# Kernel optimization log

Hardware: AMD Instinct MI355X
Metric: run time of the kernel (lower is better)

Reference implementation:

```python
import jax, jax.numpy as jnp
import numpy as np

N_NODES = 50000
N_EDGES = 800000
N_GRAPHS = 512
NODE_IN = 128
EDGE_IN = 64
HIDDEN = 128
SHARED = 64


def setup_inputs() -> dict:
    key = jax.random.key(0)
    ks = jax.random.split(key, 24)
    def lin(k, fan_in, fan_out):
        lim = 1.0 / np.sqrt(fan_in)
        kw, kb = jax.random.split(k)
        w = jax.random.uniform(kw, (fan_in, fan_out), jnp.float32, -lim, lim)
        b = jax.random.uniform(kb, (fan_out,), jnp.float32, -lim, lim)
        return w, b
    x = jax.random.normal(ks[0], (N_NODES, NODE_IN), jnp.float32)
    edge_index = jax.random.randint(ks[1], (2, N_EDGES), 0, N_NODES, jnp.int64)
    edge_attr = jax.random.normal(ks[2], (N_EDGES, EDGE_IN), jnp.float32)
    batch = jnp.sort(jax.random.randint(ks[3], (N_NODES,), 0, N_GRAPHS, jnp.int64))
    e1_w, e1_b = lin(ks[4], EDGE_IN, NODE_IN)
    n1_w1, n1_b1 = lin(ks[5], NODE_IN, HIDDEN)
    n1_w2, n1_b2 = lin(ks[6], HIDDEN, HIDDEN)
    e2_w, e2_b = lin(ks[7], EDGE_IN, HIDDEN)
    n2_w1, n2_b1 = lin(ks[8], HIDDEN, HIDDEN)
    n2_w2, n2_b2 = lin(ks[9], HIDDEN, HIDDEN)
    fc_w, fc_b = lin(ks[10], HIDDEN, SHARED)
    hS_w, hS_b = lin(ks[11], SHARED, 1)
    hP_w, hP_b = lin(ks[12], SHARED, 1)
    hN_w, hN_b = lin(ks[13], SHARED, 1)
    return dict(x=x, edge_index=edge_index, edge_attr=edge_attr, batch=batch,
                e1_w=e1_w, e1_b=e1_b, n1_w1=n1_w1, n1_b1=n1_b1, n1_w2=n1_w2, n1_b2=n1_b2,
                e2_w=e2_w, e2_b=e2_b, n2_w1=n2_w1, n2_b1=n2_b1, n2_w2=n2_w2, n2_b2=n2_b2,
                fc_w=fc_w, fc_b=fc_b, hS_w=hS_w, hS_b=hS_b, hP_w=hP_w, hP_b=hP_b,
                hN_w=hN_w, hN_b=hN_b)


def gine_conv(x, edge_index, edge_attr, ew, eb, w1, b1, w2, b2):
    # message: relu(x_j + Lin(edge_attr)); aggregate: scatter-sum to target;
    # update: MLP((1 + eps) * x_i + aggr) with eps = 0 (PyG default)
    e = edge_attr @ ew + eb                      # [E, C]
    m = jax.nn.relu(x[edge_index[0]] + e)        # gather + fused add/relu
    aggr = jax.ops.segment_sum(m, edge_index[1], num_segments=N_NODES)
    h = x + aggr
    return jax.nn.relu(h @ w1 + b1) @ w2 + b2


def global_mean_pool(x, batch):
    sums = jax.ops.segment_sum(x, batch, num_segments=N_GRAPHS)
    cnt = jax.ops.segment_sum(jnp.ones((x.shape[0],), x.dtype), batch, num_segments=N_GRAPHS)
    return sums / jnp.maximum(cnt, 1.0)[:, None]


def reference(x, edge_index, edge_attr, batch,
              e1_w, e1_b, n1_w1, n1_b1, n1_w2, n1_b2,
              e2_w, e2_b, n2_w1, n2_b1, n2_w2, n2_b2,
              fc_w, fc_b, hS_w, hS_b, hP_w, hP_b, hN_w, hN_b):
    h = jax.nn.relu(gine_conv(x, edge_index, edge_attr, e1_w, e1_b, n1_w1, n1_b1, n1_w2, n1_b2))
    h = jax.nn.relu(gine_conv(h, edge_index, edge_attr, e2_w, e2_b, n2_w1, n2_b1, n2_w2, n2_b2))
    g = global_mean_pool(h, batch)               # [G, HIDDEN]
    s = jax.nn.relu(g @ fc_w + fc_b)             # [G, SHARED]
    logS = (s @ hS_w + hS_b)[:, 0]
    logP = (s @ hP_w + hP_b)[:, 0]
    nr = (s @ hN_w + hN_b)[:, 0]
    return logS, logP, nr
```

## Files before the change

kernel.cpp:

```cpp
#include <hip/hip_runtime.h>
#include <hip/hip_bf16.h>


typedef __bf16 bf16_t;

#define N_NODES   50000
#define N_EDGES   800000
#define N_GRAPHS  512
#define HID       128
#define EIN       64

#define RL(v, l) __int_as_float(__builtin_amdgcn_readlane(__float_as_int(v), (l)))

__device__ __forceinline__ float ldf(const void* p, size_t i, int f32m) {
    return f32m ? ((const float*)p)[i] : (float)((const bf16_t*)p)[i];
}
__device__ __forceinline__ int ldi(const void* p, size_t i, int i64m) {
    return i64m ? (int)((const long long*)p)[i] : ((const int*)p)[i];
}

__global__ void k_detect(const unsigned short* __restrict__ xw,
                         const unsigned int*   __restrict__ eiw,
                         int* __restrict__ flags)
{
    if (threadIdx.x == 0 && blockIdx.x == 0) {
        int sane = 0;
        for (int i = 0; i < 256; ++i) {
            int e = (xw[i] >> 7) & 0xFF;
            if (e >= 100 && e <= 150) ++sane;
        }
        flags[0] = (sane < 220) ? 1 : 0;
        int nzhigh = 0;
        for (int i = 0; i < 256; ++i)
            if (eiw[2*i + 1] != 0) ++nzhigh;
        flags[1] = (nzhigh == 0) ? 1 : 0;
    }
}

__global__ void k_cvt4(const void* __restrict__ x, float* __restrict__ dst,
                       const int* __restrict__ flags) {
    const int f32m = flags[0];
    size_t i = (size_t)blockIdx.x * 256 + threadIdx.x;
    if (f32m) {
        ((float4*)dst)[i] = ((const float4*)x)[i];
    } else {
        const bf16_t* s = (const bf16_t*)x;
        float4 v;
        v.x = (float)s[4*i+0]; v.y = (float)s[4*i+1];
        v.z = (float)s[4*i+2]; v.w = (float)s[4*i+3];
        ((float4*)dst)[i] = v;
    }
}

__global__ __launch_bounds__(512) void k_edge_s(
        const void* __restrict__ Xg, int xg_ws,
        const void* __restrict__ ei,
        const void* __restrict__ ea,
        const void* __restrict__ ew,
        const void* __restrict__ eb,
        float*      __restrict__ ag,
        const int*  __restrict__ flags)
{
    __shared__ float4 Wq[16 * 128];
    __shared__ float  ebs[HID];
    const int f32m = flags[0];
    const int i64m = flags[1];
    const int xgf  = xg_ws ? 1 : f32m;

    for (int i = threadIdx.x; i < 16 * 128; i += 512) {
        int k4 = i >> 7, c = i & 127;
        float4 w;
        w.x = ldf(ew, (size_t)(4*k4+0)*HID + c, f32m);
        w.y = ldf(ew, (size_t)(4*k4+1)*HID + c, f32m);
        w.z = ldf(ew, (size_t)(4*k4+2)*HID + c, f32m);
        w.w = ldf(ew, (size_t)(4*k4+3)*HID + c, f32m);
        Wq[i] = w;
    }
    for (int i = threadIdx.x; i < HID; i += 512) ebs[i] = ldf(eb, i, f32m);
    __syncthreads();

    const int lane = threadIdx.x & 63;
    const int wid  = (blockIdx.x * 512 + threadIdx.x) >> 6;
    const int nw   = gridDim.x * 8;
    const int ngrp = N_EDGES / 8;

    for (int g = wid; g < ngrp; g += nw) {
        const int e0 = g * 8;
        float av[8]; int src[8], dst[8];
#pragma unroll
        for (int i = 0; i < 8; ++i) {
            av[i]  = ldf(ea, (size_t)(e0+i) * EIN + lane, f32m);
            src[i] = ldi(ei, e0+i, i64m);
            dst[i] = ldi(ei, (size_t)N_EDGES + e0+i, i64m);
        }
        float acc0[8], acc1[8];
#pragma unroll
        for (int i = 0; i < 8; ++i) { acc0[i] = 0.f; acc1[i] = 0.f; }

#pragma unroll 4
        for (int k4 = 0; k4 < 16; ++k4) {
            float4 w0 = Wq[k4 * 128 + lane];
            float4 w1 = Wq[k4 * 128 + 64 + lane];
#pragma unroll
            for (int i = 0; i < 8; ++i) {
                float a0 = RL(av[i], 4*k4+0);
                float a1 = RL(av[i], 4*k4+1);
                float a2 = RL(av[i], 4*k4+2);
                float a3 = RL(av[i], 4*k4+3);
                acc0[i] = fmaf(a3, w0.w, fmaf(a2, w0.z, fmaf(a1, w0.y, fmaf(a0, w0.x, acc0[i]))));
                acc1[i] = fmaf(a3, w1.w, fmaf(a2, w1.z, fmaf(a1, w1.y, fmaf(a0, w1.x, acc1[i]))));
            }
        }

#pragma unroll
        for (int i = 0; i < 8; ++i) {
            float x0 = ldf(Xg, (size_t)src[i] * HID + lane,      xgf);
            float x1 = ldf(Xg, (size_t)src[i] * HID + 64 + lane, xgf);
            float v0 = fmaxf(x0 + acc0[i] + ebs[lane],      0.f);
            float v1 = fmaxf(x1 + acc1[i] + ebs[64 + lane], 0.f);
            unsafeAtomicAdd(ag + (size_t)dst[i] * HID + lane,      v0);
            unsafeAtomicAdd(ag + (size_t)dst[i] * HID + 64 + lane, v1);
        }
    }
}

__global__ __launch_bounds__(1024) void k_mlp_s(
        const float* __restrict__ A,
        const void*  __restrict__ W,
        const void*  __restrict__ bias,
        float*       __restrict__ Out,
        float*       __restrict__ Out2,
        const int*   __restrict__ flags)
{
    __shared__ float4 Wq[32 * 128];
    const int f32m = flags[0];
    for (int i = threadIdx.x; i < 32 * 128; i += 1024) {
        int k4 = i >> 7, c = i & 127;
        float4 w;
        w.x = ldf(W, (size_t)(4*k4+0)*HID + c, f32m);
        w.y = ldf(W, (size_t)(4*k4+1)*HID + c, f32m);
        w.z = ldf(W, (size_t)(4*k4+2)*HID + c, f32m);
        w.w = ldf(W, (size_t)(4*k4+3)*HID + c, f32m);
        Wq[i] = w;
    }
    __syncthreads();

    const int lane = threadIdx.x & 63;
    const int wid  = (blockIdx.x * 1024 + threadIdx.x) >> 6;
    const int nw   = gridDim.x * 16;
    const float b0 = ldf(bias, lane,      f32m);
    const float b1 = ldf(bias, 64 + lane, f32m);
    const int ngrp = N_NODES / 8;

    for (int g = wid; g < ngrp; g += nw) {
        const int n0 = g * 8;
        float alo[8], ahi[8], acc0[8], acc1[8];
#pragma unroll
        for (int i = 0; i < 8; ++i) {
            alo[i] = A[(size_t)(n0+i) * HID + lane];
            ahi[i] = A[(size_t)(n0+i) * HID + 64 + lane];
            acc0[i] = b0; acc1[i] = b1;
        }
#pragma unroll 4
        for (int k4 = 0; k4 < 16; ++k4) {
            float4 w0 = Wq[k4 * 128 + lane];
            float4 w1 = Wq[k4 * 128 + 64 + lane];
#pragma unroll
            for (int i = 0; i < 8; ++i) {
                float a0 = RL(alo[i], 4*k4+0);
                float a1 = RL(alo[i], 4*k4+1);
                float a2 = RL(alo[i], 4*k4+2);
                float a3 = RL(alo[i], 4*k4+3);
                acc0[i] = fmaf(a3, w0.w, fmaf(a2, w0.z, fmaf(a1, w0.y, fmaf(a0, w0.x, acc0[i]))));
                acc1[i] = fmaf(a3, w1.w, fmaf(a2, w1.z, fmaf(a1, w1.y, fmaf(a0, w1.x, acc1[i]))));
            }
        }
#pragma unroll 4
        for (int k4 = 16; k4 < 32; ++k4) {
            float4 w0 = Wq[k4 * 128 + lane];
            float4 w1 = Wq[k4 * 128 + 64 + lane];
#pragma unroll
            for (int i = 0; i < 8; ++i) {
                float a0 = RL(ahi[i], 4*k4+0 - 64);
                float a1 = RL(ahi[i], 4*k4+1 - 64);
                float a2 = RL(ahi[i], 4*k4+2 - 64);
                float a3 = RL(ahi[i], 4*k4+3 - 64);
                acc0[i] = fmaf(a3, w0.w, fmaf(a2, w0.z, fmaf(a1, w0.y, fmaf(a0, w0.x, acc0[i]))));
                acc1[i] = fmaf(a3, w1.w, fmaf(a2, w1.z, fmaf(a1, w1.y, fmaf(a0, w1.x, acc1[i]))));
            }
        }
#pragma unroll
        for (int i = 0; i < 8; ++i) {
            float v0 = fmaxf(acc0[i], 0.f);
            float v1 = fmaxf(acc1[i], 0.f);
            Out[(size_t)(n0+i) * HID + lane]      = v0;
            Out[(size_t)(n0+i) * HID + 64 + lane] = v1;
            if (Out2) {
                Out2[(size_t)(n0+i) * HID + lane]      = v0;
                Out2[(size_t)(n0+i) * HID + 64 + lane] = v1;
            }
        }
    }
}

__global__ void k_pool_s(const float* __restrict__ X, const void* __restrict__ batch,
                         float* __restrict__ GS, float* __restrict__ GC,
                         const int* __restrict__ flags)
{
    const int i64m = flags[1];
    const int c  = threadIdx.x;
    const int n0 = blockIdx.x * 64;
    const int nend = (n0 + 64 < N_NODES) ? n0 + 64 : N_NODES;

    int bprev = ldi(batch, n0, i64m);
    float acc = 0.f;
    int   cnt = 0;
    for (int n = n0; n < nend; ++n) {
        int b = ldi(batch, n, i64m);
        if (b != bprev) {
            unsafeAtomicAdd(&GS[(size_t)bprev * HID + c], acc);
            if (c == 0) unsafeAtomicAdd(&GC[bprev], (float)cnt);
            acc = 0.f; cnt = 0; bprev = b;
        }
        acc += X[(size_t)n * HID + c];
        ++cnt;
    }
    unsafeAtomicAdd(&GS[(size_t)bprev * HID + c], acc);
    if (c == 0) unsafeAtomicAdd(&GC[bprev], (float)cnt);
}

__global__ void k_head(const float* __restrict__ GS, const float* __restrict__ GC,
                       const void* __restrict__ fcw, const void* __restrict__ fcb,
                       const void* __restrict__ hSw, const void* __restrict__ hSb,
                       const void* __restrict__ hPw, const void* __restrict__ hPb,
                       const void* __restrict__ hNw, const void* __restrict__ hNb,
                       float* __restrict__ out, const int* __restrict__ flags)
{
    const int f32m = flags[0];
    const int g = blockIdx.x;
    const int lane = threadIdx.x;
    const float inv = 1.f / fmaxf(GC[g], 1.f);
    const float g0 = GS[(size_t)g * HID + lane]      * inv;
    const float g1 = GS[(size_t)g * HID + 64 + lane] * inv;

    float acc = 0.f;
    for (int k = 0; k < 64; ++k) {
        float gk = __shfl(g0, k, 64);
        acc += gk * ldf(fcw, k * 64 + lane, f32m);
    }
    for (int k = 0; k < 64; ++k) {
        float gk = __shfl(g1, k, 64);
        acc += gk * ldf(fcw, (64 + k) * 64 + lane, f32m);
    }
    float s = fmaxf(acc + ldf(fcb, lane, f32m), 0.f);

    float pS = s * ldf(hSw, lane, f32m);
    float pP = s * ldf(hPw, lane, f32m);
    float pN = s * ldf(hNw, lane, f32m);
#pragma unroll
    for (int off = 32; off; off >>= 1) {
        pS += __shfl_down(pS, off, 64);
        pP += __shfl_down(pP, off, 64);
        pN += __shfl_down(pN, off, 64);
    }
    if (lane == 0) {
        out[g]                = pS + ldf(hSb, 0, f32m);
        out[N_GRAPHS + g]     = pP + ldf(hPb, 0, f32m);
        out[2 * N_GRAPHS + g] = pN + ldf(hNb, 0, f32m);
    }
}

extern "C" void kernel_launch(void* const* d_in, const int* in_sizes, int n_in,
                              void* d_out, int out_size, void* d_ws, size_t ws_size,
                              hipStream_t stream)
{
    const void* x     = d_in[0];
    const void* ei    = d_in[1];
    const void* ea    = d_in[2];
    const void* batch = d_in[3];
    const void* e1w = d_in[4],  *e1b = d_in[5];
    const void* n1w1= d_in[6],  *n1b1= d_in[7];
    const void* n1w2= d_in[8],  *n1b2= d_in[9];
    const void* e2w = d_in[10], *e2b = d_in[11];
    const void* n2w1= d_in[12], *n2b1= d_in[13];
    const void* n2w2= d_in[14], *n2b2= d_in[15];
    const void* fcw = d_in[16], *fcb = d_in[17];
    const void* hSw = d_in[18], *hSb = d_in[19];
    const void* hPw = d_in[20], *hPb = d_in[21];
    const void* hNw = d_in[22], *hNb = d_in[23];

    float* B1 = (float*)d_ws;
    float* B2 = B1 + (size_t)N_NODES * HID;
    float* GS = B2 + (size_t)N_NODES * HID;
    float* GC = GS + (size_t)N_GRAPHS * HID;
    int*   FL = (int*)(GC + N_GRAPHS);

    k_detect<<<1, 64, 0, stream>>>((const unsigned short*)x, (const unsigned int*)ei, FL);
    hipMemsetAsync(GS, 0, (N_GRAPHS * HID + N_GRAPHS) * sizeof(float), stream);

    const int NV4_BLKS = (N_NODES * HID / 4) / 256;

    k_cvt4  <<<NV4_BLKS, 256, 0, stream>>>(x, B1, FL);
    k_edge_s<<<1024, 512, 0, stream>>>(x, 0, ei, ea, e1w, e1b, B1, FL);
    k_mlp_s <<<512, 1024, 0, stream>>>(B1, n1w1, n1b1, B1, nullptr, FL);
    k_mlp_s <<<512, 1024, 0, stream>>>(B1, n1w2, n1b2, B1, B2, FL);

    k_edge_s<<<1024, 512, 0, stream>>>(B1, 1, ei, ea, e2w, e2b, B2, FL);
    k_mlp_s <<<512, 1024, 0, stream>>>(B2, n2w1, n2b1, B2, nullptr, FL);
    k_mlp_s <<<512, 1024, 0, stream>>>(B2, n2w2, n2b2, B2, nullptr, FL);

    k_pool_s<<<(N_NODES + 63) / 64, 128, 0, stream>>>(B2, batch, GS, GC, FL);
    k_head  <<<N_GRAPHS, 64, 0, stream>>>(GS, GC, fcw, fcb, hSw, hSb, hPw, hPb, hNw, hNb,
                                          (float*)d_out, FL);
}
```

Before: 1.283 ms.

## Replace atomic edge scatter with CSR-by-destination gather aggregation

Builds a destination-sorted CSR (histogram, three-stage scan, scatter of edge id and source) each call, then aggregates messages per node in registers and writes each node row once. This removes the float atomics on the aggregation buffer, the x-to-buffer conversion kernel and the duplicate output copy in the MLP. In exchange it adds several small preprocessing kernels with int atomics, random gathers of edge_attr rows through an indirection, and wave-level load imbalance from varying node degree.

```diff
diff --git a/kernel.cpp b/kernel.cpp
--- a/kernel.cpp
+++ b/kernel.cpp
@@ -9,6 +9,8 @@
 #define N_GRAPHS  512
 #define HID       128
 #define EIN       64
+#define SCAN_BLK  1024
+#define NCHUNK    49
 
 #define RL(v, l) __int_as_float(__builtin_amdgcn_readlane(__float_as_int(v), (l)))
 
@@ -37,34 +39,84 @@
     }
 }
 
-__global__ void k_cvt4(const void* __restrict__ x, float* __restrict__ dst,
-                       const int* __restrict__ flags) {
-    const int f32m = flags[0];
-    size_t i = (size_t)blockIdx.x * 256 + threadIdx.x;
-    if (f32m) {
-        ((float4*)dst)[i] = ((const float4*)x)[i];
-    } else {
-        const bf16_t* s = (const bf16_t*)x;
-        float4 v;
-        v.x = (float)s[4*i+0]; v.y = (float)s[4*i+1];
-        v.z = (float)s[4*i+2]; v.w = (float)s[4*i+3];
-        ((float4*)dst)[i] = v;
-    }
-}
-
-__global__ __launch_bounds__(512) void k_edge_s(
+__global__ void k_hist(const void* __restrict__ ei, int* __restrict__ CNT,
+                       const int* __restrict__ flags)
+{
+    const int i64m = flags[1];
+    int e = blockIdx.x * 256 + threadIdx.x;
+    int d = ldi(ei, (size_t)N_EDGES + e, i64m);
+    atomicAdd(&CNT[d], 1);
+}
+
+__global__ __launch_bounds__(SCAN_BLK) void k_scanA(const int* __restrict__ CNT,
+                                                    int* __restrict__ OFF,
+                                                    int* __restrict__ PS)
+{
+    __shared__ int tmp[SCAN_BLK];
+    const int t = threadIdx.x;
+    const int i = blockIdx.x * SCAN_BLK + t;
+    const int v = (i < N_NODES) ? CNT[i] : 0;
+    tmp[t] = v;
+    __syncthreads();
+    for (int off = 1; off < SCAN_BLK; off <<= 1) {
+        int u = (t >= off) ? tmp[t - off] : 0;
+        __syncthreads();
+        tmp[t] += u;
+        __syncthreads();
+    }
+    if (i < N_NODES) OFF[i] = tmp[t] - v;
+    if (t == SCAN_BLK - 1) PS[blockIdx.x] = tmp[t];
+}
+
+__global__ void k_scanB(int* __restrict__ PS)
+{
+    const int lane = threadIdx.x;
+    const int v0 = (lane < NCHUNK) ? PS[lane] : 0;
+    int v = v0;
+#pragma unroll
+    for (int off = 1; off < 64; off <<= 1) {
+        int u = __shfl_up(v, off, 64);
+        if (lane >= off) v += u;
+    }
+    if (lane < NCHUNK) PS[lane] = v - v0;
+}
+
+__global__ void k_scanC(int* __restrict__ OFF, const int* __restrict__ PS,
+                        int* __restrict__ CUR)
+{
+    int i = blockIdx.x * 256 + threadIdx.x;
+    if (i < N_NODES) {
+        int o = OFF[i] + PS[i >> 10];
+        OFF[i] = o;
+        CUR[i] = o;
+    }
+}
+
+__global__ void k_scatter(const void* __restrict__ ei, int* __restrict__ CUR,
+                          int2* __restrict__ ES, const int* __restrict__ flags)
+{
+    const int i64m = flags[1];
+    int e = blockIdx.x * 256 + threadIdx.x;
+    int s = ldi(ei, e, i64m);
+    int d = ldi(ei, (size_t)N_EDGES + e, i64m);
+    int p = atomicAdd(&CUR[d], 1);
+    ES[p] = make_int2(e, s);
+}
+
+__global__ __launch_bounds__(512) void k_edge_csr(
         const void* __restrict__ Xg, int xg_ws,
-        const void* __restrict__ ei,
+        const int2* __restrict__ ES,
+        const int*  __restrict__ OFF,
+        const int*  __restrict__ CNT,
         const void* __restrict__ ea,
         const void* __restrict__ ew,
         const void* __restrict__ eb,
-        float*      __restrict__ ag,
+        float*      __restrict__ out,
         const int*  __restrict__ flags)
 {
     __shared__ float4 Wq[16 * 128];
     __shared__ float  ebs[HID];
     const int f32m = flags[0];
-    const int i64m = flags[1];
     const int xgf  = xg_ws ? 1 : f32m;
 
     for (int i = threadIdx.x; i < 16 * 128; i += 512) {
@@ -82,45 +134,53 @@
     const int lane = threadIdx.x & 63;
     const int wid  = (blockIdx.x * 512 + threadIdx.x) >> 6;
     const int nw   = gridDim.x * 8;
-    const int ngrp = N_EDGES / 8;
-
-    for (int g = wid; g < ngrp; g += nw) {
-        const int e0 = g * 8;
-        float av[8]; int src[8], dst[8];
-#pragma unroll
-        for (int i = 0; i < 8; ++i) {
-            av[i]  = ldf(ea, (size_t)(e0+i) * EIN + lane, f32m);
-            src[i] = ldi(ei, e0+i, i64m);
-            dst[i] = ldi(ei, (size_t)N_EDGES + e0+i, i64m);
-        }
-        float acc0[8], acc1[8];
-#pragma unroll
-        for (int i = 0; i < 8; ++i) { acc0[i] = 0.f; acc1[i] = 0.f; }
+    const float eb0 = ebs[lane], eb1 = ebs[64 + lane];
+
+    for (int n = wid; n < N_NODES; n += nw) {
+        const int st = OFF[n];
+        const int d  = CNT[n];
+        float a0 = ldf(Xg, (size_t)n * HID + lane,      xgf);
+        float a1 = ldf(Xg, (size_t)n * HID + 64 + lane, xgf);
+
+        for (int base = 0; base < d; base += 8) {
+            const int m = d - base;
+            float av[8]; int src[8];
+#pragma unroll
+            for (int i = 0; i < 8; ++i) {
+                int2 es = ES[st + base + ((i < m) ? i : 0)];
+                src[i] = es.y;
+                av[i]  = ldf(ea, (size_t)es.x * EIN + lane, f32m);
+            }
+            float macc0[8], macc1[8];
+#pragma unroll
+            for (int i = 0; i < 8; ++i) { macc0[i] = 0.f; macc1[i] = 0.f; }
 
 #pragma unroll 4
-        for (int k4 = 0; k4 < 16; ++k4) {
-            float4 w0 = Wq[k4 * 128 + lane];
-            float4 w1 = Wq[k4 * 128 + 64 + lane];
+            for (int k4 = 0; k4 < 16; ++k4) {
+                float4 w0 = Wq[k4 * 128 + lane];
+                float4 w1 = Wq[k4 * 128 + 64 + lane];
+#pragma unroll
+                for (int i = 0; i < 8; ++i) {
+                    float a0b = RL(av[i], 4*k4+0);
+                    float a1b = RL(av[i], 4*k4+1);
+                    float a2b = RL(av[i], 4*k4+2);
+                    float a3b = RL(av[i], 4*k4+3);
+                    macc0[i] = fmaf(a3b, w0.w, fmaf(a2b, w0.z, fmaf(a1b, w0.y, fmaf(a0b, w0.x, macc0[i]))));
+                    macc1[i] = fmaf(a3b, w1.w, fmaf(a2b, w1.z, fmaf(a1b, w1.y, fmaf(a0b, w1.x, macc1[i]))));
+                }
+            }
 #pragma unroll
             for (int i = 0; i < 8; ++i) {
-                float a0 = RL(av[i], 4*k4+0);
-                float a1 = RL(av[i], 4*k4+1);
-                float a2 = RL(av[i], 4*k4+2);
-                float a3 = RL(av[i], 4*k4+3);
-                acc0[i] = fmaf(a3, w0.w, fmaf(a2, w0.z, fmaf(a1, w0.y, fmaf(a0, w0.x, acc0[i]))));
-                acc1[i] = fmaf(a3, w1.w, fmaf(a2, w1.z, fmaf(a1, w1.y, fmaf(a0, w1.x, acc1[i]))));
-            }
-        }
-
-#pragma unroll
-        for (int i = 0; i < 8; ++i) {
-            float x0 = ldf(Xg, (size_t)src[i] * HID + lane,      xgf);
-            float x1 = ldf(Xg, (size_t)src[i] * HID + 64 + lane, xgf);
-            float v0 = fmaxf(x0 + acc0[i] + ebs[lane],      0.f);
-            float v1 = fmaxf(x1 + acc1[i] + ebs[64 + lane], 0.f);
-            unsafeAtomicAdd(ag + (size_t)dst[i] * HID + lane,      v0);
-            unsafeAtomicAdd(ag + (size_t)dst[i] * HID + 64 + lane, v1);
-        }
+                if (i < m) {
+                    float x0 = ldf(Xg, (size_t)src[i] * HID + lane,      xgf);
+                    float x1 = ldf(Xg, (size_t)src[i] * HID + 64 + lane, xgf);
+                    a0 += fmaxf(x0 + macc0[i] + eb0, 0.f);
+                    a1 += fmaxf(x1 + macc1[i] + eb1, 0.f);
+                }
+            }
+        }
+        out[(size_t)n * HID + lane]      = a0;
+        out[(size_t)n * HID + 64 + lane] = a1;
     }
 }
 
@@ -129,7 +189,6 @@
         const void*  __restrict__ W,
         const void*  __restrict__ bias,
         float*       __restrict__ Out,
-        float*       __restrict__ Out2,
         const int*   __restrict__ flags)
 {
     __shared__ float4 Wq[32 * 128];
@@ -191,14 +250,8 @@
         }
 #pragma unroll
         for (int i = 0; i < 8; ++i) {
-            float v0 = fmaxf(acc0[i], 0.f);
-            float v1 = fmaxf(acc1[i], 0.f);
-            Out[(size_t)(n0+i) * HID + lane]      = v0;
-            Out[(size_t)(n0+i) * HID + 64 + lane] = v1;
-            if (Out2) {
-                Out2[(size_t)(n0+i) * HID + lane]      = v0;
-                Out2[(size_t)(n0+i) * HID + 64 + lane] = v1;
-            }
+            Out[(size_t)(n0+i) * HID + lane]      = fmaxf(acc0[i], 0.f);
+            Out[(size_t)(n0+i) * HID + 64 + lane] = fmaxf(acc1[i], 0.f);
         }
     }
 }
@@ -289,25 +342,34 @@
     const void* hPw = d_in[20], *hPb = d_in[21];
     const void* hNw = d_in[22], *hNb = d_in[23];
 
-    float* B1 = (float*)d_ws;
-    float* B2 = B1 + (size_t)N_NODES * HID;
-    float* GS = B2 + (size_t)N_NODES * HID;
-    float* GC = GS + (size_t)N_GRAPHS * HID;
-    int*   FL = (int*)(GC + N_GRAPHS);
+    float* B1  = (float*)d_ws;
+    float* B2  = B1 + (size_t)N_NODES * HID;
+    float* GS  = B2 + (size_t)N_NODES * HID;
+    float* GC  = GS + (size_t)N_GRAPHS * HID;
+    int*   FL  = (int*)(GC + N_GRAPHS);
+    int*   PS  = FL + 4;
+    int*   OFF = PS + 64;
+    int*   CNT = OFF + N_NODES;
+    int*   CUR = CNT + N_NODES;
+    int2*  ES  = (int2*)(CUR + N_NODES);
 
     k_detect<<<1, 64, 0, stream>>>((const unsigned short*)x, (const unsigned int*)ei, FL);
     hipMemsetAsync(GS, 0, (N_GRAPHS * HID + N_GRAPHS) * sizeof(float), stream);
-
-    const int NV4_BLKS = (N_NODES * HID / 4) / 256;
-
-    k_cvt4  <<<NV4_BLKS, 256, 0, stream>>>(x, B1, FL);
-    k_edge_s<<<1024, 512, 0, stream>>>(x, 0, ei, ea, e1w, e1b, B1, FL);
-    k_mlp_s <<<512, 1024, 0, stream>>>(B1, n1w1, n1b1, B1, nullptr, FL);
-    k_mlp_s <<<512, 1024, 0, stream>>>(B1, n1w2, n1b2, B1, B2, FL);
-
-    k_edge_s<<<1024, 512, 0, stream>>>(B1, 1, ei, ea, e2w, e2b, B2, FL);
-    k_mlp_s <<<512, 1024, 0, stream>>>(B2, n2w1, n2b1, B2, nullptr, FL);
-    k_mlp_s <<<512, 1024, 0, stream>>>(B2, n2w2, n2b2, B2, nullptr, FL);
+    hipMemsetAsync(CNT, 0, N_NODES * sizeof(int), stream);
+
+    k_hist   <<<N_EDGES / 256, 256, 0, stream>>>(ei, CNT, FL);
+    k_scanA  <<<NCHUNK, SCAN_BLK, 0, stream>>>(CNT, OFF, PS);
+    k_scanB  <<<1, 64, 0, stream>>>(PS);
+    k_scanC  <<<(N_NODES + 255) / 256, 256, 0, stream>>>(OFF, PS, CUR);
+    k_scatter<<<N_EDGES / 256, 256, 0, stream>>>(ei, CUR, ES, FL);
+
+    k_edge_csr<<<1024, 512, 0, stream>>>(x, 0, ES, OFF, CNT, ea, e1w, e1b, B1, FL);
+    k_mlp_s   <<<512, 1024, 0, stream>>>(B1, n1w1, n1b1, B1, FL);
+    k_mlp_s   <<<512, 1024, 0, stream>>>(B1, n1w2, n1b2, B1, FL);
+
+    k_edge_csr<<<1024, 512, 0, stream>>>(B1, 1, ES, OFF, CNT, ea, e2w, e2b, B2, FL);
+    k_mlp_s   <<<512, 1024, 0, stream>>>(B2, n2w1, n2b1, B2, FL);
+    k_mlp_s   <<<512, 1024, 0, stream>>>(B2, n2w2, n2b2, B2, FL);
 
     k_pool_s<<<(N_NODES + 63) / 64, 128, 0, stream>>>(B2, batch, GS, GC, FL);
     k_head  <<<N_GRAPHS, 64, 0, stream>>>(GS, GC, fcw, fcb, hSw, hSb, hPw, hPb, hNw, hNb,
```

After: 1.614 ms. 25.8% more time.

## Software-pipeline edge kernel loads, broadcast indices via readlane, shrink pool chunks

Applied to the files above, without the earlier changes.

The edge kernel now prefetches the next edge group's attributes and indices while computing the current one. Instead of every lane loading all 16 indices, one lane per index loads it and readlane broadcasts it. The source-node gathers are issued before the matmul so their latency overlaps the FMAs, and the edge grid doubles to 2048 blocks. The pool kernel uses 16-node chunks with lane-loaded batch ids, giving more blocks at the cost of extra register pressure and more atomics.

```diff
diff --git a/kernel.cpp b/kernel.cpp
--- a/kernel.cpp
+++ b/kernel.cpp
@@ -9,8 +9,10 @@
 #define N_GRAPHS  512
 #define HID       128
 #define EIN       64
-
-#define RL(v, l) __int_as_float(__builtin_amdgcn_readlane(__float_as_int(v), (l)))
+#define PNODES    16
+
+#define RL(v, l)  __int_as_float(__builtin_amdgcn_readlane(__float_as_int(v), (l)))
+#define RLI(v, l) __builtin_amdgcn_readlane((v), (l))
 
 __device__ __forceinline__ float ldf(const void* p, size_t i, int f32m) {
     return f32m ? ((const float*)p)[i] : (float)((const bf16_t*)p)[i];
@@ -83,43 +85,86 @@
     const int wid  = (blockIdx.x * 512 + threadIdx.x) >> 6;
     const int nw   = gridDim.x * 8;
     const int ngrp = N_EDGES / 8;
-
-    for (int g = wid; g < ngrp; g += nw) {
-        const int e0 = g * 8;
-        float av[8]; int src[8], dst[8];
-#pragma unroll
-        for (int i = 0; i < 8; ++i) {
-            av[i]  = ldf(ea, (size_t)(e0+i) * EIN + lane, f32m);
-            src[i] = ldi(ei, e0+i, i64m);
-            dst[i] = ldi(ei, (size_t)N_EDGES + e0+i, i64m);
-        }
-        float acc0[8], acc1[8];
-#pragma unroll
-        for (int i = 0; i < 8; ++i) { acc0[i] = 0.f; acc1[i] = 0.f; }
+    const float eb0 = ebs[lane], eb1 = ebs[64 + lane];
+
+    auto LOADIDX = [&](int e0) -> int {
+        int v = 0;
+        if (lane < 16) {
+            size_t idx = (lane < 8) ? (size_t)(e0 + lane)
+                                    : (size_t)N_EDGES + (e0 + lane - 8);
+            v = ldi(ei, idx, i64m);
+        }
+        return v;
+    };
+
+    int g = wid;
+    if (g < ngrp) {
+        float avA[8]; int vvA;
+        {
+            const int e0 = g * 8;
+            vvA = LOADIDX(e0);
+#pragma unroll
+            for (int i = 0; i < 8; ++i)
+                avA[i] = ldf(ea, (size_t)(e0+i) * EIN + lane, f32m);
+        }
+
+        while (true) {
+            const int gB = g + nw;
+            const bool hasB = (gB < ngrp);
+            float avB[8]; int vvB = 0;
+            if (hasB) {
+                const int e0B = gB * 8;
+                vvB = LOADIDX(e0B);
+#pragma unroll
+                for (int i = 0; i < 8; ++i)
+                    avB[i] = ldf(ea, (size_t)(e0B+i) * EIN + lane, f32m);
+            }
+
+            int src[8], dst[8];
+#pragma unroll
+            for (int i = 0; i < 8; ++i) {
+                src[i] = RLI(vvA, i);
+                dst[i] = RLI(vvA, 8 + i);
+            }
+            float x0[8], x1[8];
+#pragma unroll
+            for (int i = 0; i < 8; ++i) {
+                x0[i] = ldf(Xg, (size_t)src[i] * HID + lane,      xgf);
+                x1[i] = ldf(Xg, (size_t)src[i] * HID + 64 + lane, xgf);
+            }
+
+            float acc0[8], acc1[8];
+#pragma unroll
+            for (int i = 0; i < 8; ++i) { acc0[i] = 0.f; acc1[i] = 0.f; }
 
 #pragma unroll 4
-        for (int k4 = 0; k4 < 16; ++k4) {
-            float4 w0 = Wq[k4 * 128 + lane];
-            float4 w1 = Wq[k4 * 128 + 64 + lane];
-#pragma unroll
-            for (int i = 0; i < 8; ++i) {
-                float a0 = RL(av[i], 4*k4+0);
-                float a1 = RL(av[i], 4*k4+1);
-                float a2 = RL(av[i], 4*k4+2);
-                float a3 = RL(av[i], 4*k4+3);
-                acc0[i] = fmaf(a3, w0.w, fmaf(a2, w0.z, fmaf(a1, w0.y, fmaf(a0, w0.x, acc0[i]))));
-                acc1[i] = fmaf(a3, w1.w, fmaf(a2, w1.z, fmaf(a1, w1.y, fmaf(a0, w1.x, acc1[i]))));
-            }
-        }
-
-#pragma unroll
-        for (int i = 0; i < 8; ++i) {
-            float x0 = ldf(Xg, (size_t)src[i] * HID + lane,      xgf);
-            float x1 = ldf(Xg, (size_t)src[i] * HID + 64 + lane, xgf);
-            float v0 = fmaxf(x0 + acc0[i] + ebs[lane],      0.f);
-            float v1 = fmaxf(x1 + acc1[i] + ebs[64 + lane], 0.f);
-            unsafeAtomicAdd(ag + (size_t)dst[i] * HID + lane,      v0);
-            unsafeAtomicAdd(ag + (size_t)dst[i] * HID + 64 + lane, v1);
+            for (int k4 = 0; k4 < 16; ++k4) {
+                float4 w0 = Wq[k4 * 128 + lane];
+                float4 w1 = Wq[k4 * 128 + 64 + lane];
+#pragma unroll
+                for (int i = 0; i < 8; ++i) {
+                    float a0 = RL(avA[i], 4*k4+0);
+                    float a1 = RL(avA[i], 4*k4+1);
+                    float a2 = RL(avA[i], 4*k4+2);
+                    float a3 = RL(avA[i], 4*k4+3);
+                    acc0[i] = fmaf(a3, w0.w, fmaf(a2, w0.z, fmaf(a1, w0.y, fmaf(a0, w0.x, acc0[i]))));
+                    acc1[i] = fmaf(a3, w1.w, fmaf(a2, w1.z, fmaf(a1, w1.y, fmaf(a0, w1.x, acc1[i]))));
+                }
+            }
+
+#pragma unroll
+            for (int i = 0; i < 8; ++i) {
+                float v0 = fmaxf(x0[i] + acc0[i] + eb0, 0.f);
+                float v1 = fmaxf(x1[i] + acc1[i] + eb1, 0.f);
+                unsafeAtomicAdd(ag + (size_t)dst[i] * HID + lane,      v0);
+                unsafeAtomicAdd(ag + (size_t)dst[i] * HID + 64 + lane, v1);
+            }
+
+            if (!hasB) break;
+            g = gB;
+            vvA = vvB;
+#pragma unroll
+            for (int i = 0; i < 8; ++i) avA[i] = avB[i];
         }
     }
 }
@@ -209,20 +254,23 @@
 {
     const int i64m = flags[1];
     const int c  = threadIdx.x;
-    const int n0 = blockIdx.x * 64;
-    const int nend = (n0 + 64 < N_NODES) ? n0 + 64 : N_NODES;
-
-    int bprev = ldi(batch, n0, i64m);
+    const int tl = threadIdx.x & 63;
+    const int n0 = blockIdx.x * PNODES;
+
+    int bv = (tl < PNODES) ? ldi(batch, n0 + tl, i64m) : 0;
+
+    int bprev = RLI(bv, 0);
     float acc = 0.f;
     int   cnt = 0;
-    for (int n = n0; n < nend; ++n) {
-        int b = ldi(batch, n, i64m);
+#pragma unroll
+    for (int j = 0; j < PNODES; ++j) {
+        int b = RLI(bv, j);
         if (b != bprev) {
             unsafeAtomicAdd(&GS[(size_t)bprev * HID + c], acc);
             if (c == 0) unsafeAtomicAdd(&GC[bprev], (float)cnt);
             acc = 0.f; cnt = 0; bprev = b;
         }
-        acc += X[(size_t)n * HID + c];
+        acc += X[(size_t)(n0 + j) * HID + c];
         ++cnt;
     }
     unsafeAtomicAdd(&GS[(size_t)bprev * HID + c], acc);
@@ -301,15 +349,15 @@
     const int NV4_BLKS = (N_NODES * HID / 4) / 256;
 
     k_cvt4  <<<NV4_BLKS, 256, 0, stream>>>(x, B1, FL);
-    k_edge_s<<<1024, 512, 0, stream>>>(x, 0, ei, ea, e1w, e1b, B1, FL);
+    k_edge_s<<<2048, 512, 0, stream>>>(x, 0, ei, ea, e1w, e1b, B1, FL);
     k_mlp_s <<<512, 1024, 0, stream>>>(B1, n1w1, n1b1, B1, nullptr, FL);
     k_mlp_s <<<512, 1024, 0, stream>>>(B1, n1w2, n1b2, B1, B2, FL);
 
-    k_edge_s<<<1024, 512, 0, stream>>>(B1, 1, ei, ea, e2w, e2b, B2, FL);
+    k_edge_s<<<2048, 512, 0, stream>>>(B1, 1, ei, ea, e2w, e2b, B2, FL);
     k_mlp_s <<<512, 1024, 0, stream>>>(B2, n2w1, n2b1, B2, nullptr, FL);
     k_mlp_s <<<512, 1024, 0, stream>>>(B2, n2w2, n2b2, B2, nullptr, FL);
 
-    k_pool_s<<<(N_NODES + 63) / 64, 128, 0, stream>>>(B2, batch, GS, GC, FL);
+    k_pool_s<<<N_NODES / PNODES, 128, 0, stream>>>(B2, batch, GS, GC, FL);
     k_head  <<<N_GRAPHS, 64, 0, stream>>>(GS, GC, fcw, fcb, hSw, hSb, hPw, hPb, hNw, hNb,
                                           (float*)d_out, FL);
 }
```

New measurement: 1.224 ms. 1.05x faster.
